# Kernel optimization log

Measured on AMD Instinct MI355X. Metric: run time of the kernel, lower is better.

## Reference

```python
import jax, jax.numpy as jnp
import numpy as np

B, S, D, H, F = 4, 2048, 512, 8, 2048
HD = D // H
SCALE = HD ** -0.5


def layernorm(x, g, b, eps=1e-5):
    mu = jnp.mean(x, axis=-1, keepdims=True)
    var = jnp.var(x, axis=-1, keepdims=True)
    return (x - mu) * jax.lax.rsqrt(var + eps) * g + b


def setup_inputs() -> dict:
    key = jax.random.key(0)
    ks = jax.random.split(key, 10)
    s = 0.02
    return {
        "x": jax.random.normal(ks[0], (B, S, D), jnp.float32),
        "w_qkv": jax.random.normal(ks[1], (D, 3 * D), jnp.float32) * s,
        "b_qkv": jnp.zeros((3 * D,), jnp.float32),
        "w_o": jax.random.normal(ks[2], (D, D), jnp.float32) * s,
        "b_o": jnp.zeros((D,), jnp.float32),
        "w1": jax.random.normal(ks[3], (D, F), jnp.float32) * s,
        "b1": jnp.zeros((F,), jnp.float32),
        "w2": jax.random.normal(ks[4], (F, D), jnp.float32) * s,
        "b2": jnp.zeros((D,), jnp.float32),
        "g1": jnp.ones((D,), jnp.float32),
        "be1": jnp.zeros((D,), jnp.float32),
        "g2": jnp.ones((D,), jnp.float32),
        "be2": jnp.zeros((D,), jnp.float32),
    }


def reference(x, w_qkv, b_qkv, w_o, b_o, w1, b1, w2, b2, g1, be1, g2, be2):
    res = x
    qkv = x @ w_qkv + b_qkv                       # [B,S,3D]
    q, k, v = jnp.split(qkv, 3, axis=-1)          # each [B,S,D]
    # head partition: [B,S,D] -> [B,H,S,hd]
    def split_heads(t):
        return t.reshape(B, S, H, HD).transpose(0, 2, 1, 3)
    q, k, v = map(split_heads, (q, k, v))
    scores = jnp.einsum('bhqc,bhkc->bhqk', q, k) * SCALE
    weights = jax.nn.softmax(scores, axis=-1)
    out = jnp.einsum('bhqk,bhkc->bhqc', weights, v)
    out = out.transpose(0, 2, 1, 3).reshape(B, S, D)  # merge heads
    out = out @ w_o + b_o
    out = layernorm(out + res, g1, be1)
    res = out
    out = jax.nn.gelu(out @ w1 + b1, approximate=False) @ w2 + b2
    out = layernorm(out + res, g2, be2)
    return out
```

## Files before the change

kernel.cpp:

```cpp
#include <hip/hip_runtime.h>
#include <math.h>

constexpr int B = 4, S = 2048, D = 512, H = 8, HD = 64, F = 2048;
constexpr int M = B * S;
constexpr float C_QK = 0.125f * 1.44269504088896340736f;

typedef __bf16 bf16x8 __attribute__((ext_vector_type(8)));
typedef float  f32x4  __attribute__((ext_vector_type(4)));
typedef float  f32x16 __attribute__((ext_vector_type(16)));

static __device__ __forceinline__ short f2bf(float f) {
  return __builtin_bit_cast(short, (__bf16)f);
}

static __device__ __forceinline__ void gload16(const void* g, void* l) {
  __builtin_amdgcn_global_load_lds(
      (const __attribute__((address_space(1))) unsigned int*)g,
      (__attribute__((address_space(3))) unsigned int*)l, 16, 0, 0);
}

__global__ __launch_bounds__(256)
void prep_all(const float* __restrict__ x, short* __restrict__ xb,
              const float* __restrict__ w_qkv, short* __restrict__ wtq,
              const float* __restrict__ w_o,  short* __restrict__ wto,
              const float* __restrict__ w1,   short* __restrict__ wt1,
              const float* __restrict__ w2,   short* __restrict__ wt2) {
  __shared__ float tl[32][33];
  const int id = blockIdx.x;
  const int t = threadIdx.x;
  if (id < 4096) {
    int i = id * 256 + t;
    float4 v = ((const float4*)x)[i];
    ((short4*)xb)[i] = make_short4(f2bf(v.x), f2bf(v.y), f2bf(v.z), f2bf(v.w));
    return;
  }
  const float* in; short* out; int R, C, bx, by;
  if (id < 4864)      { int k = id - 4096; in = w_qkv; out = wtq; R = 512;  C = 1536; bx = k % 48; by = k / 48; }
  else if (id < 5120) { int k = id - 4864; in = w_o;   out = wto; R = 512;  C = 512;  bx = k % 16; by = k / 16; }
  else if (id < 6144) { int k = id - 5120; in = w1;    out = wt1; R = 512;  C = 2048; bx = k % 64; by = k / 64; }
  else                { int k = id - 6144; in = w2;    out = wt2; R = 2048; C = 512;  bx = k % 16; by = k / 16; }
  const int r0 = by * 32, c0 = bx * 32;
  const int tr = t >> 3, tc4 = (t & 7) * 4;
  float4 v = *(const float4*)&in[(size_t)(r0 + tr) * C + c0 + tc4];
  tl[tr][tc4] = v.x; tl[tr][tc4 + 1] = v.y; tl[tr][tc4 + 2] = v.z; tl[tr][tc4 + 3] = v.w;
  __syncthreads();
  short4 o = make_short4(f2bf(tl[tc4][tr]), f2bf(tl[tc4 + 1][tr]),
                         f2bf(tl[tc4 + 2][tr]), f2bf(tl[tc4 + 3][tr]));
  *(short4*)&out[(size_t)(c0 + tr) * R + r0 + tc4] = o;
}

template<int GELU, int EPI>
__global__ __launch_bounds__(256)
void gemm_bf16(const short* __restrict__ A, const short* __restrict__ Wt,
               const float* __restrict__ bias,
               float* __restrict__ Cf, short* __restrict__ Cb,
               short* __restrict__ qsw, short* __restrict__ ksw,
               short* __restrict__ vsw, int K, int N) {
  __shared__ short As[2][128 * 64] __attribute__((aligned(16)));
  __shared__ short Bs[2][128 * 64] __attribute__((aligned(16)));
  const int t = threadIdx.x;
  const int w = t >> 6, l = t & 63, g = l >> 4, r = l & 15;
  const int wm = w >> 1, wn = w & 1;
  const int m0 = blockIdx.y * 128, n0 = blockIdx.x * 128;

#define STAGE_TILE(buf, k0)                                                     \
  {                                                                             \
    _Pragma("unroll")                                                           \
    for (int iss = 0; iss < 4; ++iss) {                                         \
      int q = iss * 256 + t;                                                    \
      int row = q >> 3, sl = (q & 7) ^ (row & 7);                               \
      gload16(A + (size_t)(m0 + row) * K + (k0) + sl * 8,                       \
              (char*)As[buf] + q * 16);                                         \
    }                                                                           \
    _Pragma("unroll")                                                           \
    for (int iss = 0; iss < 4; ++iss) {                                         \
      int q = iss * 256 + t;                                                    \
      int row = q >> 3, sl = (q & 7) ^ (row & 7);                               \
      gload16(Wt + (size_t)(n0 + row) * K + (k0) + sl * 8,                      \
              (char*)Bs[buf] + q * 16);                                         \
    }                                                                           \
  }

  f32x4 acc[4][4] = {};
  const int NS = K >> 6;
  STAGE_TILE(0, 0);
  __syncthreads();
  for (int st = 0; st < NS; ++st) {
    const int cur = st & 1;
    if (st + 1 < NS) STAGE_TILE(cur ^ 1, (st + 1) << 6);
    const short* Ac = As[cur];
    const short* Bc = Bs[cur];
#pragma unroll
    for (int kh = 0; kh < 2; ++kh) {
      const int cc = kh * 4 + g;
      bf16x8 aF[4], bF[4];
#pragma unroll
      for (int mi = 0; mi < 4; ++mi) {
        const int row = wm * 64 + mi * 16 + r;
        aF[mi] = *(const bf16x8*)(Ac + row * 64 + ((cc ^ (r & 7)) << 3));
      }
#pragma unroll
      for (int ni = 0; ni < 4; ++ni) {
        const int row = wn * 64 + ni * 16 + r;
        bF[ni] = *(const bf16x8*)(Bc + row * 64 + ((cc ^ (r & 7)) << 3));
      }
#pragma unroll
      for (int mi = 0; mi < 4; ++mi)
#pragma unroll
        for (int ni = 0; ni < 4; ++ni)
          acc[mi][ni] = __builtin_amdgcn_mfma_f32_16x16x32_bf16(aF[mi], bF[ni], acc[mi][ni], 0, 0, 0);
    }
    __syncthreads();
  }
#undef STAGE_TILE

#pragma unroll
  for (int mi = 0; mi < 4; ++mi) {
#pragma unroll
    for (int ni = 0; ni < 4; ++ni) {
      const int n  = n0 + wn * 64 + ni * 16 + r;
      const int mB = m0 + wm * 64 + mi * 16 + g * 4;
      float vals[4];
#pragma unroll
      for (int j = 0; j < 4; ++j) {
        float v = acc[mi][ni][j] + bias[n];
        if (GELU) v = 0.5f * v * (1.0f + erff(v * 0.70710678118654752f));
        vals[j] = v;
      }
      if (EPI == 0) {
#pragma unroll
        for (int j = 0; j < 4; ++j) Cf[(size_t)(mB + j) * N + n] = vals[j];
      } else if (EPI == 1) {
#pragma unroll
        for (int j = 0; j < 4; ++j) Cb[(size_t)(mB + j) * N + n] = f2bf(vals[j]);
      } else {
        const int b = mB >> 11, s = mB & 2047;
        if (n < 512) {
          const int hh = n >> 6, d = n & 63;
          const size_t rb = (size_t)(b * 8 + hh) * 2048;
#pragma unroll
          for (int j = 0; j < 4; ++j)
            qsw[(rb + s + j) * 64 + (d ^ (((s + j) & 7) << 3))] = f2bf(vals[j] * C_QK);
        } else if (n < 1024) {
          const int hh = (n - 512) >> 6, d = (n - 512) & 63;
          const size_t rb = (size_t)(b * 8 + hh) * 2048;
#pragma unroll
          for (int j = 0; j < 4; ++j)
            ksw[(rb + s + j) * 64 + (d ^ (((s + j) & 7) << 3))] = f2bf(vals[j]);
        } else {
          const int hh = (n - 1024) >> 6, d = (n - 1024) & 63;
          short4 pk = make_short4(f2bf(vals[0]), f2bf(vals[1]), f2bf(vals[2]), f2bf(vals[3]));
          *(short4*)&vsw[(size_t)((b * 8 + hh) * 64 + d) * 2048 + (s ^ ((d & 7) << 3))] = pk;
        }
      }
    }
  }
}

__global__ __launch_bounds__(256)
void attn_mfma(const short* __restrict__ qsw, const short* __restrict__ ksw,
               const short* __restrict__ vsw, short* __restrict__ attn_o) {
  __shared__ short Qs[128 * 64] __attribute__((aligned(16)));
  __shared__ short Ks[2][64 * 64] __attribute__((aligned(16)));
  __shared__ short Vs[2][64 * 64] __attribute__((aligned(16)));
  const int t = threadIdx.x;
  const int w = t >> 6, l = t & 63;
  const int c = l & 31, hi = l >> 5;
  const int bh = blockIdx.y;
  const int q0 = blockIdx.x * 128;
  const short* qb = qsw + ((size_t)bh * 2048 + q0) * 64;
  const short* kb = ksw + (size_t)bh * 2048 * 64;
  const short* vb = vsw + (size_t)bh * 64 * 2048;

#define STAGE_KV(buf, kt)                                                       \
  {                                                                             \
    _Pragma("unroll")                                                           \
    for (int iss = 0; iss < 2; ++iss) {                                         \
      int q = iss * 256 + t;                                                    \
      gload16(kb + (size_t)((kt) + (q >> 3)) * 64 + (q & 7) * 8,                \
              (char*)Ks[buf] + q * 16);                                         \
    }                                                                           \
    _Pragma("unroll")                                                           \
    for (int iss = 0; iss < 2; ++iss) {                                         \
      int q = iss * 256 + t;                                                    \
      gload16(vb + (size_t)(q >> 3) * 2048 + (kt) + (q & 7) * 8,                \
              (char*)Vs[buf] + q * 16);                                         \
    }                                                                           \
  }

#pragma unroll
  for (int iss = 0; iss < 4; ++iss) {
    int q = iss * 256 + t;
    gload16(qb + (q >> 3) * 64 + (q & 7) * 8, (char*)Qs + q * 16);
  }
  STAGE_KV(0, 0);
  __syncthreads();

  const int qrow = w * 32 + c;
  const int swz = (c & 7) << 3;
  bf16x8 qf[4];
#pragma unroll
  for (int dc = 0; dc < 4; ++dc)
    qf[dc] = *(const bf16x8*)(Qs + qrow * 64 + ((dc * 16 + hi * 8) ^ swz));

  f32x16 o0 = {}, o1 = {};
  float m_run = -3e38f, l_run = 0.0f;

  for (int ti = 0; ti < 32; ++ti) {
    const int cur = ti & 1;
    if (ti < 31) STAGE_KV(cur ^ 1, (ti + 1) * 64);
    const short* Kc = Ks[cur];
    const short* Vc = Vs[cur];

    f32x16 s0 = {}, s1 = {};
    __builtin_amdgcn_s_setprio(1);
#pragma unroll
    for (int dc = 0; dc < 4; ++dc) {
      const int koff = (dc * 16 + hi * 8) ^ swz;
      bf16x8 kf0 = *(const bf16x8*)(Kc + c * 64 + koff);
      bf16x8 kf1 = *(const bf16x8*)(Kc + (32 + c) * 64 + koff);
      s0 = __builtin_amdgcn_mfma_f32_32x32x16_bf16(kf0, qf[dc], s0, 0, 0, 0);
      s1 = __builtin_amdgcn_mfma_f32_32x32x16_bf16(kf1, qf[dc], s1, 0, 0, 0);
    }
    __builtin_amdgcn_s_setprio(0);

    float tmax = -3e38f;
#pragma unroll
    for (int j = 0; j < 16; ++j) tmax = fmaxf(tmax, fmaxf(s0[j], s1[j]));
    tmax = fmaxf(tmax, __shfl_xor(tmax, 32, 64));
    if (__any(tmax - m_run > 8.0f)) {
      float mnew = fmaxf(m_run, tmax);
      float rs = __builtin_amdgcn_exp2f(m_run - mnew);
      m_run = mnew;
      l_run *= rs;
#pragma unroll
      for (int j = 0; j < 16; ++j) {
        float rj = __shfl(rs, (j & 3) + 8 * (j >> 2) + 4 * hi, 64);
        o0[j] *= rj; o1[j] *= rj;
      }
    }
    float rsum = 0.0f;
#pragma unroll
    for (int j = 0; j < 16; ++j) {
      s0[j] = __builtin_amdgcn_exp2f(s0[j] - m_run);
      s1[j] = __builtin_amdgcn_exp2f(s1[j] - m_run);
      rsum += s0[j] + s1[j];
    }
    rsum += __shfl_xor(rsum, 32, 64);
    l_run += rsum;

    __builtin_amdgcn_s_setprio(1);
#pragma unroll
    for (int kc = 0; kc < 4; ++kc) {
      const int jb = (kc & 1) * 8;
      int u0, u1, v0, v1;
      if (kc < 2) {
        asm("v_cvt_pk_bf16_f32 %0, %1, %2" : "=v"(u0) : "v"(s0[jb + 0]), "v"(s0[jb + 1]));
        asm("v_cvt_pk_bf16_f32 %0, %1, %2" : "=v"(u1) : "v"(s0[jb + 2]), "v"(s0[jb + 3]));
        asm("v_cvt_pk_bf16_f32 %0, %1, %2" : "=v"(v0) : "v"(s0[jb + 4]), "v"(s0[jb + 5]));
        asm("v_cvt_pk_bf16_f32 %0, %1, %2" : "=v"(v1) : "v"(s0[jb + 6]), "v"(s0[jb + 7]));
      } else {
        asm("v_cvt_pk_bf16_f32 %0, %1, %2" : "=v"(u0) : "v"(s1[jb + 0]), "v"(s1[jb + 1]));
        asm("v_cvt_pk_bf16_f32 %0, %1, %2" : "=v"(u1) : "v"(s1[jb + 2]), "v"(s1[jb + 3]));
        asm("v_cvt_pk_bf16_f32 %0, %1, %2" : "=v"(v0) : "v"(s1[jb + 4]), "v"(s1[jb + 5]));
        asm("v_cvt_pk_bf16_f32 %0, %1, %2" : "=v"(v1) : "v"(s1[jb + 6]), "v"(s1[jb + 7]));
      }
      asm volatile("v_permlane32_swap_b32 %0, %1" : "+v"(u0), "+v"(v0));
      asm volatile("v_permlane32_swap_b32 %0, %1" : "+v"(u1), "+v"(v1));
      int pw[4] = {u0, u1, v0, v1};
      bf16x8 pa = __builtin_bit_cast(bf16x8, *(int4*)pw);
      const int voff = (kc * 16 + hi * 8) ^ swz;
      bf16x8 vf0 = *(const bf16x8*)(Vc + c * 64 + voff);
      bf16x8 vf1 = *(const bf16x8*)(Vc + (32 + c) * 64 + voff);
      o0 = __builtin_amdgcn_mfma_f32_32x32x16_bf16(pa, vf0, o0, 0, 0, 0);
      o1 = __builtin_amdgcn_mfma_f32_32x32x16_bf16(pa, vf1, o1, 0, 0, 0);
    }
    __builtin_amdgcn_s_setprio(0);
    __syncthreads();
  }
#undef STAGE_KV

  const int b = bh >> 3, hh = bh & 7;
  float inv = 1.0f / l_run;
#pragma unroll
  for (int j = 0; j < 16; ++j) {
    const int q_rel = (j & 3) + 8 * (j >> 2) + 4 * hi;
    float invq = __shfl(inv, q_rel, 64);
    const size_t row = (size_t)(b * 2048 + q0 + w * 32 + q_rel) * 512 + hh * 64;
    attn_o[row + c]      = f2bf(o0[j] * invq);
    attn_o[row + 32 + c] = f2bf(o1[j] * invq);
  }
}

template<int WB>
__global__ __launch_bounds__(256)
void add_ln(const float* __restrict__ a, const float* __restrict__ res,
            const float* __restrict__ g_, const float* __restrict__ be,
            float* __restrict__ out, short* __restrict__ outb) {
  const int row = blockIdx.x;
  const int t = threadIdx.x;
  const size_t off = (size_t)row * D;
  float x0 = a[off + t] + res[off + t];
  float x1 = a[off + t + 256] + res[off + t + 256];
  float sum = x0 + x1;
  float sq  = x0 * x0 + x1 * x1;
#pragma unroll
  for (int o2 = 32; o2 > 0; o2 >>= 1) {
    sum += __shfl_down(sum, o2);
    sq  += __shfl_down(sq, o2);
  }
  __shared__ float ssum[4], ssq[4];
  const int wid = t >> 6;
  if ((t & 63) == 0) { ssum[wid] = sum; ssq[wid] = sq; }
  __syncthreads();
  if (t == 0) {
    ssum[0] = ssum[0] + ssum[1] + ssum[2] + ssum[3];
    ssq[0]  = ssq[0] + ssq[1] + ssq[2] + ssq[3];
  }
  __syncthreads();
  float mu   = ssum[0] * (1.0f / D);
  float var  = ssq[0] * (1.0f / D) - mu * mu;
  float rstd = rsqrtf(var + 1e-5f);
  float y0 = (x0 - mu) * rstd * g_[t] + be[t];
  float y1 = (x1 - mu) * rstd * g_[t + 256] + be[t + 256];
  out[off + t] = y0;
  out[off + t + 256] = y1;
  if (WB) {
    outb[off + t] = f2bf(y0);
    outb[off + t + 256] = f2bf(y1);
  }
}

extern "C" void kernel_launch(void* const* d_in, const int* in_sizes, int n_in,
                              void* d_out, int out_size, void* d_ws, size_t ws_size,
                              hipStream_t stream) {
  const float* x     = (const float*)d_in[0];
  const float* w_qkv = (const float*)d_in[1];
  const float* b_qkv = (const float*)d_in[2];
  const float* w_o   = (const float*)d_in[3];
  const float* b_o   = (const float*)d_in[4];
  const float* w1    = (const float*)d_in[5];
  const float* b1    = (const float*)d_in[6];
  const float* w2    = (const float*)d_in[7];
  const float* b2    = (const float*)d_in[8];
  const float* g1    = (const float*)d_in[9];
  const float* be1   = (const float*)d_in[10];
  const float* g2    = (const float*)d_in[11];
  const float* be2   = (const float*)d_in[12];
  float* out = (float*)d_out;
  (void)in_sizes; (void)n_in; (void)out_size; (void)ws_size;

  const size_t MD = (size_t)M * 512;
  short* q_sw = (short*)d_ws;
  short* k_sw = q_sw + MD;
  short* v_sw = k_sw + MD;
  short* a_o  = v_sw + MD;
  short* h    = q_sw;
  short* xb   = a_o + MD;
  short* ln1b = xb;
  short* wtq  = xb + MD;
  short* wto  = wtq + (size_t)1536 * 512;
  short* wt1  = wto + (size_t)512 * 512;
  short* wt2  = wt1 + (size_t)512 * 2048;
  float* buf  = (float*)(wt2 + (size_t)2048 * 512);
  float* ln1  = buf + MD;

  prep_all<<<7168, 256, 0, stream>>>(x, xb, w_qkv, wtq, w_o, wto, w1, wt1, w2, wt2);

  gemm_bf16<0, 2><<<dim3(12, 64), 256, 0, stream>>>(
      xb, wtq, b_qkv, nullptr, nullptr, q_sw, k_sw, v_sw, 512, 1536);
  attn_mfma<<<dim3(16, 32), 256, 0, stream>>>(q_sw, k_sw, v_sw, a_o);
  gemm_bf16<0, 0><<<dim3(4, 64), 256, 0, stream>>>(
      a_o, wto, b_o, buf, nullptr, nullptr, nullptr, nullptr, 512, 512);
  add_ln<1><<<M, 256, 0, stream>>>(buf, x, g1, be1, ln1, ln1b);
  gemm_bf16<1, 1><<<dim3(16, 64), 256, 0, stream>>>(
      ln1b, wt1, b1, nullptr, h, nullptr, nullptr, nullptr, 512, 2048);
  gemm_bf16<0, 0><<<dim3(4, 64), 256, 0, stream>>>(
      h, wt2, b2, buf, nullptr, nullptr, nullptr, nullptr, 2048, 512);
  add_ln<0><<<M, 256, 0, stream>>>(buf, ln1, g2, be2, out, nullptr);
}
```

Baseline: 294.8 us.

## Split attention over key halves with combine kernel and shrink GEMM tiles

Attention now runs as a split-K (flash-decoding style) launch over two key halves. Each half writes bf16 partial outputs plus a log-sum-exp, and a new combine kernel merges them into the head-merged layout. Q fragments are read straight from global memory instead of staged through LDS. The GEMM is templated on tile size, with smaller tiles (128x64, 64x64) for every projection to raise block count and occupancy across the CUs. The cost is an extra kernel launch, extra global traffic for the partials, bf16 rounding of the partial outputs, and less data reuse per GEMM tile.

```diff
diff --git a/kernel.cpp b/kernel.cpp
--- a/kernel.cpp
+++ b/kernel.cpp
@@ -49,77 +49,74 @@
   *(short4*)&out[(size_t)(c0 + tr) * R + r0 + tc4] = o;
 }
 
-template<int GELU, int EPI>
+template<int BM, int BN, int GELU, int EPI>
 __global__ __launch_bounds__(256)
 void gemm_bf16(const short* __restrict__ A, const short* __restrict__ Wt,
                const float* __restrict__ bias,
                float* __restrict__ Cf, short* __restrict__ Cb,
                short* __restrict__ qsw, short* __restrict__ ksw,
                short* __restrict__ vsw, int K, int N) {
-  __shared__ short As[2][128 * 64] __attribute__((aligned(16)));
-  __shared__ short Bs[2][128 * 64] __attribute__((aligned(16)));
+  constexpr int MI = BM / 32, NI = BN / 32;
+  __shared__ short As[2][BM * 64] __attribute__((aligned(16)));
+  __shared__ short Bs[2][BN * 64] __attribute__((aligned(16)));
   const int t = threadIdx.x;
   const int w = t >> 6, l = t & 63, g = l >> 4, r = l & 15;
   const int wm = w >> 1, wn = w & 1;
-  const int m0 = blockIdx.y * 128, n0 = blockIdx.x * 128;
-
-#define STAGE_TILE(buf, k0)                                                     \
-  {                                                                             \
-    _Pragma("unroll")                                                           \
-    for (int iss = 0; iss < 4; ++iss) {                                         \
-      int q = iss * 256 + t;                                                    \
-      int row = q >> 3, sl = (q & 7) ^ (row & 7);                               \
-      gload16(A + (size_t)(m0 + row) * K + (k0) + sl * 8,                       \
-              (char*)As[buf] + q * 16);                                         \
-    }                                                                           \
-    _Pragma("unroll")                                                           \
-    for (int iss = 0; iss < 4; ++iss) {                                         \
-      int q = iss * 256 + t;                                                    \
-      int row = q >> 3, sl = (q & 7) ^ (row & 7);                               \
-      gload16(Wt + (size_t)(n0 + row) * K + (k0) + sl * 8,                      \
-              (char*)Bs[buf] + q * 16);                                         \
-    }                                                                           \
-  }
-
-  f32x4 acc[4][4] = {};
+  const int m0 = blockIdx.y * BM, n0 = blockIdx.x * BN;
+
+  auto stage = [&](int buf, int k0) {
+#pragma unroll
+    for (int i = 0; i < BM / 32; ++i) {
+      int q = i * 256 + t;
+      int row = q >> 3, sl = (q & 7) ^ (row & 7);
+      gload16(A + (size_t)(m0 + row) * K + k0 + sl * 8, (char*)As[buf] + q * 16);
+    }
+#pragma unroll
+    for (int i = 0; i < BN / 32; ++i) {
+      int q = i * 256 + t;
+      int row = q >> 3, sl = (q & 7) ^ (row & 7);
+      gload16(Wt + (size_t)(n0 + row) * K + k0 + sl * 8, (char*)Bs[buf] + q * 16);
+    }
+  };
+
+  f32x4 acc[MI][NI] = {};
   const int NS = K >> 6;
-  STAGE_TILE(0, 0);
+  stage(0, 0);
   __syncthreads();
   for (int st = 0; st < NS; ++st) {
     const int cur = st & 1;
-    if (st + 1 < NS) STAGE_TILE(cur ^ 1, (st + 1) << 6);
+    if (st + 1 < NS) stage(cur ^ 1, (st + 1) << 6);
     const short* Ac = As[cur];
     const short* Bc = Bs[cur];
 #pragma unroll
     for (int kh = 0; kh < 2; ++kh) {
       const int cc = kh * 4 + g;
-      bf16x8 aF[4], bF[4];
-#pragma unroll
-      for (int mi = 0; mi < 4; ++mi) {
-        const int row = wm * 64 + mi * 16 + r;
+      bf16x8 aF[MI], bF[NI];
+#pragma unroll
+      for (int mi = 0; mi < MI; ++mi) {
+        const int row = wm * (MI * 16) + mi * 16 + r;
         aF[mi] = *(const bf16x8*)(Ac + row * 64 + ((cc ^ (r & 7)) << 3));
       }
 #pragma unroll
-      for (int ni = 0; ni < 4; ++ni) {
-        const int row = wn * 64 + ni * 16 + r;
+      for (int ni = 0; ni < NI; ++ni) {
+        const int row = wn * (NI * 16) + ni * 16 + r;
         bF[ni] = *(const bf16x8*)(Bc + row * 64 + ((cc ^ (r & 7)) << 3));
       }
 #pragma unroll
-      for (int mi = 0; mi < 4; ++mi)
-#pragma unroll
-        for (int ni = 0; ni < 4; ++ni)
+      for (int mi = 0; mi < MI; ++mi)
+#pragma unroll
+        for (int ni = 0; ni < NI; ++ni)
           acc[mi][ni] = __builtin_amdgcn_mfma_f32_16x16x32_bf16(aF[mi], bF[ni], acc[mi][ni], 0, 0, 0);
     }
     __syncthreads();
   }
-#undef STAGE_TILE
-
-#pragma unroll
-  for (int mi = 0; mi < 4; ++mi) {
-#pragma unroll
-    for (int ni = 0; ni < 4; ++ni) {
-      const int n  = n0 + wn * 64 + ni * 16 + r;
-      const int mB = m0 + wm * 64 + mi * 16 + g * 4;
+
+#pragma unroll
+  for (int mi = 0; mi < MI; ++mi) {
+#pragma unroll
+    for (int ni = 0; ni < NI; ++ni) {
+      const int n  = n0 + wn * (NI * 16) + ni * 16 + r;
+      const int mB = m0 + wm * (MI * 16) + mi * 16 + g * 4;
       float vals[4];
 #pragma unroll
       for (int j = 0; j < 4; ++j) {
@@ -159,8 +156,8 @@
 
 __global__ __launch_bounds__(256)
 void attn_mfma(const short* __restrict__ qsw, const short* __restrict__ ksw,
-               const short* __restrict__ vsw, short* __restrict__ attn_o) {
-  __shared__ short Qs[128 * 64] __attribute__((aligned(16)));
+               const short* __restrict__ vsw, short* __restrict__ Opart,
+               float* __restrict__ Lpart) {
   __shared__ short Ks[2][64 * 64] __attribute__((aligned(16)));
   __shared__ short Vs[2][64 * 64] __attribute__((aligned(16)));
   const int t = threadIdx.x;
@@ -168,47 +165,41 @@
   const int c = l & 31, hi = l >> 5;
   const int bh = blockIdx.y;
   const int q0 = blockIdx.x * 128;
+  const int half = blockIdx.z;
+  const int kbase = half * 1024;
   const short* qb = qsw + ((size_t)bh * 2048 + q0) * 64;
   const short* kb = ksw + (size_t)bh * 2048 * 64;
   const short* vb = vsw + (size_t)bh * 64 * 2048;
 
-#define STAGE_KV(buf, kt)                                                       \
-  {                                                                             \
-    _Pragma("unroll")                                                           \
-    for (int iss = 0; iss < 2; ++iss) {                                         \
-      int q = iss * 256 + t;                                                    \
-      gload16(kb + (size_t)((kt) + (q >> 3)) * 64 + (q & 7) * 8,                \
-              (char*)Ks[buf] + q * 16);                                         \
-    }                                                                           \
-    _Pragma("unroll")                                                           \
-    for (int iss = 0; iss < 2; ++iss) {                                         \
-      int q = iss * 256 + t;                                                    \
-      gload16(vb + (size_t)(q >> 3) * 2048 + (kt) + (q & 7) * 8,                \
-              (char*)Vs[buf] + q * 16);                                         \
-    }                                                                           \
-  }
-
-#pragma unroll
-  for (int iss = 0; iss < 4; ++iss) {
-    int q = iss * 256 + t;
-    gload16(qb + (q >> 3) * 64 + (q & 7) * 8, (char*)Qs + q * 16);
-  }
-  STAGE_KV(0, 0);
-  __syncthreads();
+  auto stage_kv = [&](int buf, int kt) {
+#pragma unroll
+    for (int i = 0; i < 2; ++i) {
+      int q = i * 256 + t;
+      gload16(kb + (size_t)(kt + (q >> 3)) * 64 + (q & 7) * 8, (char*)Ks[buf] + q * 16);
+    }
+#pragma unroll
+    for (int i = 0; i < 2; ++i) {
+      int q = i * 256 + t;
+      gload16(vb + (size_t)(q >> 3) * 2048 + kt + (q & 7) * 8, (char*)Vs[buf] + q * 16);
+    }
+  };
 
   const int qrow = w * 32 + c;
   const int swz = (c & 7) << 3;
   bf16x8 qf[4];
 #pragma unroll
   for (int dc = 0; dc < 4; ++dc)
-    qf[dc] = *(const bf16x8*)(Qs + qrow * 64 + ((dc * 16 + hi * 8) ^ swz));
+    qf[dc] = *(const bf16x8*)(qb + qrow * 64 + ((dc * 16 + hi * 8) ^ swz));
+
+  stage_kv(0, kbase);
+  __syncthreads();
 
   f32x16 o0 = {}, o1 = {};
   float m_run = -3e38f, l_run = 0.0f;
 
-  for (int ti = 0; ti < 32; ++ti) {
+  for (int ti = 0; ti < 16; ++ti) {
     const int cur = ti & 1;
-    if (ti < 31) STAGE_KV(cur ^ 1, (ti + 1) * 64);
+    if (ti < 15) stage_kv(cur ^ 1, kbase + (ti + 1) * 64);
     const short* Kc = Ks[cur];
     const short* Vc = Vs[cur];
 
@@ -278,18 +269,40 @@
     __builtin_amdgcn_s_setprio(0);
     __syncthreads();
   }
-#undef STAGE_KV
-
-  const int b = bh >> 3, hh = bh & 7;
+
+  const size_t hrow = (size_t)half * (32 * 2048) + (size_t)bh * 2048;
   float inv = 1.0f / l_run;
+  if (hi == 0)
+    Lpart[hrow + q0 + w * 32 + c] = m_run + __builtin_log2f(l_run);
 #pragma unroll
   for (int j = 0; j < 16; ++j) {
     const int q_rel = (j & 3) + 8 * (j >> 2) + 4 * hi;
     float invq = __shfl(inv, q_rel, 64);
-    const size_t row = (size_t)(b * 2048 + q0 + w * 32 + q_rel) * 512 + hh * 64;
-    attn_o[row + c]      = f2bf(o0[j] * invq);
-    attn_o[row + 32 + c] = f2bf(o1[j] * invq);
-  }
+    const size_t row = (hrow + q0 + w * 32 + q_rel) * 64;
+    Opart[row + c]      = f2bf(o0[j] * invq);
+    Opart[row + 32 + c] = f2bf(o1[j] * invq);
+  }
+}
+
+__global__ __launch_bounds__(256)
+void attn_combine(const short* __restrict__ Opart, const float* __restrict__ Lpart,
+                  short* __restrict__ a_o) {
+  const int idx = blockIdx.x * 256 + threadIdx.x;
+  const int row = idx >> 3;
+  const int d8 = (idx & 7) * 8;
+  const float L0 = Lpart[row], L1 = Lpart[65536 + row];
+  const float mx = fmaxf(L0, L1);
+  const float w0 = __builtin_amdgcn_exp2f(L0 - mx), w1 = __builtin_amdgcn_exp2f(L1 - mx);
+  const float inv = 1.0f / (w0 + w1);
+  bf16x8 a = *(const bf16x8*)(Opart + (size_t)row * 64 + d8);
+  bf16x8 b = *(const bf16x8*)(Opart + ((size_t)65536 + row) * 64 + d8);
+  bf16x8 res;
+#pragma unroll
+  for (int i = 0; i < 8; ++i)
+    res[i] = (__bf16)((w0 * (float)a[i] + w1 * (float)b[i]) * inv);
+  const int bh = row >> 11, s = row & 2047;
+  const int bb = bh >> 3, hh = bh & 7;
+  *(bf16x8*)(a_o + ((size_t)(bb * 2048 + s)) * 512 + hh * 64 + d8) = res;
 }
 
 template<int WB>
@@ -364,18 +377,21 @@
   short* wt2  = wt1 + (size_t)512 * 2048;
   float* buf  = (float*)(wt2 + (size_t)2048 * 512);
   float* ln1  = buf + MD;
+  short* Opart = (short*)(ln1 + MD);
+  float* Lpart = (float*)(Opart + (size_t)2 * 32 * 2048 * 64);
 
   prep_all<<<7168, 256, 0, stream>>>(x, xb, w_qkv, wtq, w_o, wto, w1, wt1, w2, wt2);
 
-  gemm_bf16<0, 2><<<dim3(12, 64), 256, 0, stream>>>(
+  gemm_bf16<128, 64, 0, 2><<<dim3(24, 64), 256, 0, stream>>>(
       xb, wtq, b_qkv, nullptr, nullptr, q_sw, k_sw, v_sw, 512, 1536);
-  attn_mfma<<<dim3(16, 32), 256, 0, stream>>>(q_sw, k_sw, v_sw, a_o);
-  gemm_bf16<0, 0><<<dim3(4, 64), 256, 0, stream>>>(
+  attn_mfma<<<dim3(16, 32, 2), 256, 0, stream>>>(q_sw, k_sw, v_sw, Opart, Lpart);
+  attn_combine<<<2048, 256, 0, stream>>>(Opart, Lpart, a_o);
+  gemm_bf16<64, 64, 0, 0><<<dim3(8, 128), 256, 0, stream>>>(
       a_o, wto, b_o, buf, nullptr, nullptr, nullptr, nullptr, 512, 512);
   add_ln<1><<<M, 256, 0, stream>>>(buf, x, g1, be1, ln1, ln1b);
-  gemm_bf16<1, 1><<<dim3(16, 64), 256, 0, stream>>>(
+  gemm_bf16<128, 64, 1, 1><<<dim3(32, 64), 256, 0, stream>>>(
       ln1b, wt1, b1, nullptr, h, nullptr, nullptr, nullptr, 512, 2048);
-  gemm_bf16<0, 0><<<dim3(4, 64), 256, 0, stream>>>(
+  gemm_bf16<64, 64, 0, 0><<<dim3(8, 128), 256, 0, stream>>>(
       h, wt2, b2, buf, nullptr, nullptr, nullptr, nullptr, 2048, 512);
   add_ln<0><<<M, 256, 0, stream>>>(buf, ln1, g2, be2, out, nullptr);
 }
```

Measured after the change: 295.1 us. No clear change (+0.1%).
